# Performance work log

Hardware: AMD Instinct MI355X
Metric: run time of the kernel (lower is better)

Reference implementation:

```python
import jax, jax.numpy as jnp
import numpy as np

N, IN, HID, OUT, C, H = 50000, 1488, 1024, 512, 32, 8
E = 800000

def setup_inputs() -> dict:
    key = jax.random.key(0)
    ks = jax.random.split(key, 16)
    s = lambda k, shape, fan: jax.random.normal(k, shape, jnp.float32) * (1.0 / np.sqrt(fan))
    return {
        "x": jax.random.normal(ks[0], (N, IN), jnp.float32),
        "edge_index": jax.random.randint(ks[1], (2, E), 0, N, jnp.int64),
        "ln_g": jnp.ones((IN,), jnp.float32),
        "ln_b": jnp.zeros((IN,), jnp.float32),
        "W1": s(ks[2], (IN, HID), IN), "b1": jnp.zeros((HID,), jnp.float32),
        "W2": s(ks[3], (HID, OUT), HID), "b2": jnp.zeros((OUT,), jnp.float32),
        "Wr": s(ks[4], (OUT, C * H), OUT), "br": jnp.zeros((C * H,), jnp.float32),
        "Wg": s(ks[5], (OUT, C * H), OUT),
        "att_src": s(ks[6], (H, C), C),
        "att_dst": s(ks[7], (H, C), C),
        "bg": jnp.zeros((C * H,), jnp.float32),
    }

def reference(x, edge_index, ln_g, ln_b, W1, b1, W2, b2, Wr, br, Wg, att_src, att_dst, bg):
    n = x.shape[0]
    # LayerNorm
    mu = jnp.mean(x, axis=-1, keepdims=True)
    var = jnp.mean(jnp.square(x - mu), axis=-1, keepdims=True)
    xn = (x - mu) * jax.lax.rsqrt(var + 1e-5) * ln_g + ln_b
    # init_proj MLP
    h = jax.nn.relu(xn @ W1 + b1) @ W2 + b2            # [N, OUT]
    res = h @ Wr + br                                   # [N, H*C]
    # GATConv (add_self_loops=True, dropout inactive in eval)
    loops = jnp.arange(n, dtype=edge_index.dtype)
    src = jnp.concatenate([edge_index[0], loops])
    dst = jnp.concatenate([edge_index[1], loops])
    g = (h @ Wg).reshape(n, H, C)                       # [N, H, C]
    a_src = jnp.sum(g * att_src, axis=-1)               # [N, H]
    a_dst = jnp.sum(g * att_dst, axis=-1)               # [N, H]
    e = jax.nn.leaky_relu(a_src[src] + a_dst[dst], 0.2) # [E', H]
    m = jax.ops.segment_max(e, dst, num_segments=n)     # per-dst softmax (stable)
    ex = jnp.exp(e - m[dst])
    denom = jax.ops.segment_sum(ex, dst, num_segments=n)
    alpha = ex / (denom[dst] + 1e-16)                   # [E', H]
    msg = alpha[:, :, None] * g[src]                    # [E', H, C]
    agg = jax.ops.segment_sum(msg, dst, num_segments=n) # [N, H, C]
    out = agg.reshape(n, H * C) + bg
    return jax.nn.elu(out) + res
```

## Files before the change

### kernel.cpp

```cpp
#include <hip/hip_runtime.h>
#include <hip/hip_bf16.h>
#include <cstdint>
#include <cstddef>

#define NND 50000
#define DIN 1488
#define DINP 1536
#define DHID 1024
#define DOUT 512
#define DHC 256
#define NE 800000
#define NHD 8
#define SPLITC 256

typedef __attribute__((ext_vector_type(8))) short short8;
typedef __attribute__((ext_vector_type(4))) short short4v;
typedef __attribute__((ext_vector_type(4))) float f32x4;
typedef __attribute__((ext_vector_type(4))) int int4v;
typedef unsigned short ushort_t;

__device__ __forceinline__ unsigned short f2bf(float f){
  union { float f; unsigned u; } v; v.f = f;
  unsigned r = v.u + 0x7fffu + ((v.u >> 16) & 1u);
  return (unsigned short)(r >> 16);
}
__device__ __forceinline__ float bf2f(unsigned short u){
  union { unsigned u; float f; } v; v.u = ((unsigned)u) << 16;
  return v.f;
}

__device__ __forceinline__ void async16(const void* g, void* l){
  __builtin_amdgcn_global_load_lds((__attribute__((address_space(1))) void*)g,
                                   (__attribute__((address_space(3))) void*)l, 16, 0, 0);
}

__device__ __forceinline__ void tc_tile(const float* __restrict__ W,
                                        ushort_t* __restrict__ WT,
                                        int K, int Nn, int Kp, int bx, int by){
  __shared__ float tile[32][33];
  const int tx = threadIdx.x & 31, ty = threadIdx.x >> 5;
  const int k0 = bx*32, n0 = by*32;
  for (int i = ty; i < 32; i += 8){
    int k = k0 + i, n = n0 + tx;
    tile[i][tx] = (k < K && n < Nn) ? W[(size_t)k*Nn + n] : 0.f;
  }
  __syncthreads();
  for (int i = ty; i < 32; i += 8){
    int n = n0 + i, k = k0 + tx;
    if (n < Nn && k < Kp) WT[(size_t)n*Kp + k] = f2bf(tile[tx][i]);
  }
}
__global__ __launch_bounds__(256) void prep_kernel(const float* W1, const float* Wr,
                                                   const float* Wg, const float* W2,
                                                   const float* b2, const float* br,
                                                   ushort_t* W1T, ushort_t* WrgT,
                                                   ushort_t* W2bf, float* b2rg,
                                                   int* cnt){
  int b = blockIdx.x;
  if (b < 1536){ tc_tile(W1, W1T, DIN, DHID, DINP, b % 48, b / 48); return; }
  b -= 1536;
  if (b < 128){ tc_tile(Wr, WrgT, DOUT, DHC, DOUT, b % 16, b / 16); return; }
  b -= 128;
  if (b < 128){ tc_tile(Wg, WrgT + 256*DOUT, DOUT, DHC, DOUT, b % 16, b / 16); return; }
  b -= 128;
  if (b < 256){
    const int idx = (b*256 + threadIdx.x)*8;
    f32x4 v0 = *(const f32x4*)(W2 + idx);
    f32x4 v1 = *(const f32x4*)(W2 + idx + 4);
    union { ushort_t u[8]; short8 s; } o;
    o.u[0]=f2bf(v0.x); o.u[1]=f2bf(v0.y); o.u[2]=f2bf(v0.z); o.u[3]=f2bf(v0.w);
    o.u[4]=f2bf(v1.x); o.u[5]=f2bf(v1.y); o.u[6]=f2bf(v1.z); o.u[7]=f2bf(v1.w);
    *(short8*)(W2bf + idx) = o.s;
    return;
  }
  b -= 256;
  if (b < 2){
    const int c = b*256 + threadIdx.x;
    float acc = 0.f;
    if (c < 256){
      for (int j = 0; j < DOUT; ++j) acc += b2[j]*Wr[(size_t)j*DHC + c];
      acc += br[c];
    } else {
      const int cc = c - 256;
      for (int j = 0; j < DOUT; ++j) acc += b2[j]*Wg[(size_t)j*DHC + cc];
    }
    b2rg[c] = acc;
    return;
  }
  b -= 2;
  { int i = b*256 + threadIdx.x; if (i < NND) cnt[i] = 0; }
}

#define LN_BLOCKS 12500
__global__ __launch_bounds__(256) void ln_count(const float* __restrict__ x,
                                                const float* __restrict__ gw,
                                                const float* __restrict__ bw,
                                                ushort_t* __restrict__ xn,
                                                const int* __restrict__ ei,
                                                int* __restrict__ cnt){
  const int bid = blockIdx.x;
  if (bid >= LN_BLOCKS){
    int e = (bid - LN_BLOCKS)*256 + threadIdx.x;
    if (e < NE) atomicAdd(&cnt[ei[NE + e]], 1);
    return;
  }
  const int wid = threadIdx.x >> 6, lane = threadIdx.x & 63;
  const int row = bid*4 + wid;
  if (row >= NND) return;
  const float* xr = x + (size_t)row * DIN;
  float s = 0.f, sq = 0.f;
  for (int i = lane*4; i < DIN; i += 256){
    f32x4 v = *(const f32x4*)(xr + i);
    s  += v.x + v.y + v.z + v.w;
    sq += v.x*v.x + v.y*v.y + v.z*v.z + v.w*v.w;
  }
  #pragma unroll
  for (int o = 32; o; o >>= 1){ s += __shfl_xor(s, o); sq += __shfl_xor(sq, o); }
  const float mu = s * (1.f/DIN);
  const float var = sq * (1.f/DIN) - mu*mu;
  const float rstd = rsqrtf(var + 1e-5f);
  ushort_t* xo = xn + (size_t)row * DINP;
  for (int i = lane*4; i < DIN; i += 256){
    f32x4 v = *(const f32x4*)(xr + i);
    f32x4 gg = *(const f32x4*)(gw + i);
    f32x4 bb = *(const f32x4*)(bw + i);
    union { ushort_t u[4]; unsigned long long q; } o;
    o.u[0] = f2bf((v.x-mu)*rstd*gg.x + bb.x);
    o.u[1] = f2bf((v.y-mu)*rstd*gg.y + bb.y);
    o.u[2] = f2bf((v.z-mu)*rstd*gg.z + bb.z);
    o.u[3] = f2bf((v.w-mu)*rstd*gg.w + bb.w);
    *(unsigned long long*)(xo + i) = o.q;
  }
  if (lane < (DINP - DIN)) xo[DIN + lane] = 0;
}

template<int ACT, int MODE, int CB, int SCAN>
__global__ __launch_bounds__(256, 2) void gemm128(const ushort_t* __restrict__ A,
                                                  const ushort_t* __restrict__ BT,
                                                  const float* __restrict__ bias,
                                                  void* __restrict__ out0,
                                                  void* __restrict__ out1,
                                                  int M, int Nn, int K,
                                                  const int* __restrict__ cnt,
                                                  int* __restrict__ offs,
                                                  int* __restrict__ cur){
  __shared__ __align__(16) ushort_t lds[2][2][128*64];
  const int t = threadIdx.x, wid = t >> 6, lane = t & 63;

  const int bid = blockIdx.x - SCAN, nwg = gridDim.x - SCAN;
  const int q = nwg >> 3, r = nwg & 7;
  const int xcd = bid & 7, slot = bid >> 3;
  const int lg = (xcd < r ? xcd*(q+1) : r*(q+1) + (xcd - r)*q) + slot;
  const int brow = (lg / CB) * 128, bcol = (lg % CB) * 128;

  const int l8  = t >> 3;
  const int cb  = (t & 7) << 4;
  const int scb = cb ^ ((l8 & 7) << 4);
  const ushort_t* pAr[4]; const ushort_t* pBr[4];
  #pragma unroll
  for (int rd = 0; rd < 4; ++rd){
    int ra = brow + rd*32 + l8; ra = ra < M ? ra : M-1;
    int rb = bcol + rd*32 + l8; rb = rb < Nn ? rb : Nn-1;
    pAr[rd] = A  + (size_t)ra*K + (scb >> 1);
    pBr[rd] = BT + (size_t)rb*K + (scb >> 1);
  }
  const int w8 = wid * 8;

#define STAGE1(buf, kt) do {                                           \
    const int _o = (kt) * 64;                                          \
    _Pragma("unroll")                                                  \
    for (int _rd = 0; _rd < 4; ++_rd){                                 \
      async16(pAr[_rd] + _o, &lds[buf][0][(_rd*32 + w8)*64]);          \
      async16(pBr[_rd] + _o, &lds[buf][1][(_rd*32 + w8)*64]);          \
    }                                                                  \
  } while(0)

  f32x4 acc[4][4];
  #pragma unroll
  for (int i=0;i<4;i++)
    #pragma unroll
    for (int j=0;j<4;j++) acc[i][j] = (f32x4){0.f,0.f,0.f,0.f};

  const int wr = (wid >> 1)*64, wc = (wid & 1)*64;
  const int fr = lane & 15;
  const int kb0 = (lane >> 4) << 4;
  const int sx  = (fr & 7) << 4;
  const int ko0 = ((kb0      ) ^ sx) >> 1;
  const int ko1 = ((kb0 | 64 ) ^ sx) >> 1;

  const int nk = K >> 6;
  STAGE1(0, 0);
  STAGE1(1, 1);
  for (int kt = 0; kt < nk; ++kt){
    const ushort_t* bA = lds[kt & 1][0];
    const ushort_t* bB = lds[kt & 1][1];
    if (kt + 1 < nk) asm volatile("s_waitcnt vmcnt(8)" ::: "memory");
    else             asm volatile("s_waitcnt vmcnt(0)" ::: "memory");
    __builtin_amdgcn_s_barrier();
    short8 af[4][2], bf_[4][2];
    #pragma unroll
    for (int m=0;m<4;m++){
      const int ra = (wr + m*16 + fr)*64;
      const int rb = (wc + m*16 + fr)*64;
      af[m][0]  = *(const short8*)&bA[ra + ko0];
      af[m][1]  = *(const short8*)&bA[ra + ko1];
      bf_[m][0] = *(const short8*)&bB[rb + ko0];
      bf_[m][1] = *(const short8*)&bB[rb + ko1];
    }
    asm volatile("s_waitcnt lgkmcnt(0)" ::: "memory");
    __builtin_amdgcn_sched_barrier(0);
    __builtin_amdgcn_s_barrier();
    if (kt + 2 < nk) STAGE1(kt & 1, kt + 2);
    __builtin_amdgcn_s_setprio(1);
    #pragma unroll
    for (int m=0;m<4;m++)
      #pragma unroll
      for (int n=0;n<4;n++){
        acc[m][n] = __builtin_amdgcn_mfma_f32_16x16x32_bf16(af[m][0], bf_[n][0], acc[m][n], 0, 0, 0);
        acc[m][n] = __builtin_amdgcn_mfma_f32_16x16x32_bf16(af[m][1], bf_[n][1], acc[m][n], 0, 0, 0);
      }
    __builtin_amdgcn_s_setprio(0);
  }
#undef STAGE1

  bool isf32;
  float* outF = nullptr; ushort_t* outB = nullptr; int ostride = 0, ocb = 0;
  if (MODE == 0){ isf32 = true;  outF = (float*)out0;    ostride = Nn; ocb = bcol; }
  else if (MODE == 1){ isf32 = false; outB = (ushort_t*)out0; ostride = Nn; ocb = bcol; }
  else {
    if (bcol < SPLITC){ isf32 = true;  outF = (float*)out0;    ostride = SPLITC;      ocb = bcol; }
    else              { isf32 = false; outB = (ushort_t*)out1; ostride = Nn - SPLITC; ocb = bcol - SPLITC; }
  }
  float bv[4];
  #pragma unroll
  for (int n=0;n<4;n++){
    const int col = wc + n*16 + (lane & 15);
    float b = 0.f;
    if (MODE == 2){ if (isf32 && bias) b = bias[bcol + col]; }
    else if (bias) b = bias[bcol + col];
    bv[n] = b;
  }
  float* sF = (float*)&lds[0][0][0];
  ushort_t* sB = (ushort_t*)&lds[0][0][0];
  const int trow = t >> 3, tc16 = (t & 7) * 16;
  #pragma unroll
  for (int c = 0; c < 4; ++c){
    __syncthreads();
    if ((wid >> 1) == (c >> 1)){
      #pragma unroll
      for (int mm = 0; mm < 2; ++mm){
        const int m = 2*(c & 1) + mm;
        const int rbase = m*16 + (lane >> 4)*4 - (c & 1)*32;
        #pragma unroll
        for (int n = 0; n < 4; ++n){
          const int col = wc + n*16 + (lane & 15);
          #pragma unroll
          for (int j = 0; j < 4; ++j){
            float v = acc[m][n][j] + bv[n];
            if (ACT) v = v > 0.f ? v : 0.f;
            if (isf32) sF[(rbase + j)*128 + col] = v;
            else       sB[(rbase + j)*128 + col] = f2bf(v);
          }
        }
      }
    }
    __syncthreads();
    const int grow = brow + c*32 + trow;
    if (grow < M){
      if (isf32){
        float* dst = outF + (size_t)grow*ostride + ocb + tc16;
        const float* src = sF + trow*128 + tc16;
        #pragma unroll
        for (int q2 = 0; q2 < 4; ++q2) ((f32x4*)dst)[q2] = ((const f32x4*)src)[q2];
      } else {
        ushort_t* dst = outB + (size_t)grow*ostride + ocb + tc16;
        const ushort_t* src = sB + trow*128 + tc16;
        #pragma unroll
        for (int q2 = 0; q2 < 2; ++q2) ((short8*)dst)[q2] = ((const short8*)src)[q2];
      }
    }
  }
}

template<int ACT, int CB>
__global__ __launch_bounds__(512, 1) void gemm256p8(const ushort_t* __restrict__ A,
                                                    const ushort_t* __restrict__ BT,
                                                    const float* __restrict__ bias,
                                                    ushort_t* __restrict__ out0,
                                                    int M, int Nn, int K,
                                                    const int* __restrict__ cnt,
                                                    int* __restrict__ offs,
                                                    int* __restrict__ cur){
  __shared__ __align__(16) ushort_t lds[2][2][2][64*128];
  const int t = threadIdx.x, wid = t >> 6, lane = t & 63;

  if (blockIdx.x == 0){
    int* sbuf = (int*)&lds[0][0][0][0];
    const int chunk = (NND + 255) >> 8;
    int s = 0;
    if (t < 256){
      const int s0 = t*chunk;
      const int s1 = (s0 + chunk < NND) ? s0 + chunk : NND;
      for (int i = s0; i < s1; i += 4){
        int4v v = *(const int4v*)(cnt + i);
        s += v.x + v.y + v.z + v.w + 4;
      }
    }
    sbuf[t] = s; __syncthreads();
    for (int o = 1; o < 256; o <<= 1){
      int xv = (t >= o && t < 256) ? sbuf[t-o] : 0;
      __syncthreads();
      if (t < 256) sbuf[t] += xv;
      __syncthreads();
    }
    if (t < 256){
      int run = sbuf[t] - s;
      const int s0 = t*chunk;
      const int s1 = (s0 + chunk < NND) ? s0 + chunk : NND;
      for (int i = s0; i < s1; i += 4){
        int4v v = *(const int4v*)(cnt + i);
        int4v cu;
        cu.x = run; run += v.x + 1;
        cu.y = run; run += v.y + 1;
        cu.z = run; run += v.z + 1;
        cu.w = run; run += v.w + 1;
        *(int4v*)(cur + i)  = cu;
        *(int4v*)(offs + i) = cu;
      }
      if (t == 255) offs[NND] = run;
    }
    return;
  }

  const int bid = blockIdx.x - 1, nwg = gridDim.x - 1;
  const int q = nwg >> 3, r = nwg & 7;
  const int xcd = bid & 7, slot = bid >> 3;
  const int lg = (xcd < r ? xcd*(q+1) : r*(q+1) + (xcd - r)*q) + slot;
  const int brow = (lg / CB) * 256, bcol = (lg % CB) * 256;

  const int l8  = t >> 3;
  const int cb  = (t & 7) << 4;
  const unsigned scb = (unsigned)(cb ^ ((l8 & 7) << 4));
  unsigned rowA[2][2], rowB[2][2];
  #pragma unroll
  for (int hf = 0; hf < 2; ++hf)
    #pragma unroll
    for (int rd = 0; rd < 2; ++rd){
      int ra = brow + hf*128 + rd*64 + l8; ra = ra < M ? ra : M-1;
      int rb = bcol + hf*128 + rd*64 + l8; rb = rb < Nn ? rb : Nn-1;
      rowA[hf][rd] = (unsigned)ra * (unsigned)(K*2);
      rowB[hf][rd] = (unsigned)rb * (unsigned)(K*2);
    }
  const int w8 = wid * 8;

#define STG_A(buf, hf, kt) do {                                               \
    const unsigned _ob = (unsigned)(kt)*128u + scb;                           \
    async16((const char*)A + rowA[hf][0] + _ob, &lds[buf][0][hf][(w8)*64]);   \
    async16((const char*)A + rowA[hf][1] + _ob, &lds[buf][0][hf][(64+w8)*64]);\
  } while(0)
#define STG_B(buf, hf, kt) do {                                               \
    const unsigned _ob = (unsigned)(kt)*128u + scb;                           \
    async16((const char*)BT + rowB[hf][0] + _ob, &lds[buf][1][hf][(w8)*64]);  \
    async16((const char*)BT + rowB[hf][1] + _ob, &lds[buf][1][hf][(64+w8)*64]);\
  } while(0)

  f32x4 acc[8][4];
  #pragma unroll
  for (int i=0;i<8;i++)
    #pragma unroll
    for (int j=0;j<4;j++) acc[i][j] = (f32x4){0.f,0.f,0.f,0.f};

  const int wrow = (wid >> 2), wcol = (wid & 3);
  const int fr = lane & 15;
  const int kb0 = (lane >> 4) << 4;
  const int sx  = (fr & 7) << 4;
  const int ko0 = ((kb0      ) ^ sx) >> 1;
  const int ko1 = ((kb0 | 64 ) ^ sx) >> 1;
  const int bhalf = wcol >> 1, brl = (wcol & 1)*64;

#define RD_A(buf, m) do {                                          \
    const int _ra = ((m)*16 + fr)*64;                              \
    af[m][0] = *(const short8*)&lds[buf][0][wrow][_ra + ko0];      \
    af[m][1] = *(const short8*)&lds[buf][0][wrow][_ra + ko1];      \
  } while(0)
#define RD_B(buf, n) do {                                          \
    const int _rb = (brl + (n)*16 + fr)*64;                        \
    bf[n][0] = *(const short8*)&lds[buf][1][bhalf][_rb + ko0];     \
    bf[n][1] = *(const short8*)&lds[buf][1][bhalf][_rb + ko1];     \
  } while(0)
#define SYNC_PH() do {                                             \
    __builtin_amdgcn_s_barrier();                                  \
    asm volatile("s_waitcnt lgkmcnt(0)" ::: "memory");             \
    __builtin_amdgcn_sched_barrier(0);                             \
  } while(0)
#define MFMA_Q(M0, N0) do {                                        \
    __builtin_amdgcn_s_setprio(1);                                 \
    _Pragma("unroll")                                              \
    for (int _m=(M0); _m<(M0)+4; ++_m)                             \
      _Pragma("unroll")                                            \
      for (int _n=(N0); _n<(N0)+2; ++_n){                          \
        acc[_m][_n] = __builtin_amdgcn_mfma_f32_16x16x32_bf16(af[_m][0], bf[_n][0], acc[_m][_n], 0, 0, 0); \
        acc[_m][_n] = __builtin_amdgcn_mfma_f32_16x16x32_bf16(af[_m][1], bf[_n][1], acc[_m][_n], 0, 0, 0); \
      }                                                            \
    __builtin_amdgcn_s_setprio(0);                                 \
  } while(0)

  const int nk = K >> 6;
  STG_A(0,0,0); STG_A(0,1,0); STG_B(0,0,0); STG_B(0,1,0);
  STG_A(1,0,1); STG_A(1,1,1);
  asm volatile("s_waitcnt vmcnt(4)" ::: "memory");
  __builtin_amdgcn_s_barrier();

  for (int kt = 0; kt < nk; ++kt){
    const int buf = kt & 1, obuf = buf ^ 1;
    short8 af[8][2], bf[4][2];
    RD_A(buf,0); RD_A(buf,1); RD_A(buf,2); RD_A(buf,3);
    RD_B(buf,0); RD_B(buf,1);
    if (kt + 1 < nk) STG_B(obuf, 0, kt + 1);
    SYNC_PH();
    MFMA_Q(0, 0);
    RD_A(buf,4); RD_A(buf,5); RD_A(buf,6); RD_A(buf,7);
    if (kt + 1 < nk) STG_B(obuf, 1, kt + 1);
    SYNC_PH();
    MFMA_Q(4, 0);
    RD_B(buf,2); RD_B(buf,3);
    if (kt + 2 < nk) STG_A(buf, 0, kt + 2);
    SYNC_PH();
    MFMA_Q(0, 2);
    if (kt + 2 < nk){
      STG_A(buf, 1, kt + 2);
      asm volatile("s_waitcnt vmcnt(4)" ::: "memory");
    } else {
      asm volatile("s_waitcnt vmcnt(0)" ::: "memory");
    }
    __builtin_amdgcn_s_barrier();
    MFMA_Q(4, 2);
  }
#undef STG_A
#undef STG_B
#undef RD_A
#undef RD_B
#undef SYNC_PH
#undef MFMA_Q

  float bv[4];
  #pragma unroll
  for (int n=0;n<4;n++){
    const int col = bcol + wcol*64 + n*16 + (lane & 15);
    bv[n] = bias ? bias[col] : 0.f;
  }
  ushort_t* sB = (ushort_t*)&lds[0][0][0][0];
  __syncthreads();
  #pragma unroll
  for (int m=0;m<8;m++){
    const int row = wrow*128 + m*16 + (lane >> 4)*4;
    #pragma unroll
    for (int n=0;n<4;n++){
      const int col = wcol*64 + n*16 + (lane & 15);
      #pragma unroll
      for (int j=0;j<4;j++){
        float v = acc[m][n][j] + bv[n];
        if (ACT) v = v > 0.f ? v : 0.f;
        sB[(row+j)*256 + col] = f2bf(v);
      }
    }
  }
  __syncthreads();
  const int srow = t >> 5, scol8 = (t & 31) * 8;
  #pragma unroll
  for (int rr = 0; rr < 16; ++rr){
    const int rloc = rr*16 + srow;
    const int grow = brow + rloc;
    if (grow < M)
      *(short8*)(out0 + (size_t)grow*Nn + bcol + scol8) = *(const short8*)&sB[rloc*256 + scol8];
  }
}

#define G2_NWG 392
template<int ACT, int MODE, int CB, int EXTRA>
__global__ __launch_bounds__(512, 2) void gemm256(const ushort_t* __restrict__ A,
                                                  const ushort_t* __restrict__ BT,
                                                  const float* __restrict__ bias,
                                                  void* __restrict__ out0,
                                                  void* __restrict__ out1,
                                                  int M, int Nn, int K,
                                                  const int* __restrict__ ei,
                                                  int* __restrict__ cur,
                                                  int* __restrict__ eidx,
                                                  const float* __restrict__ att_s,
                                                  const float* __restrict__ att_d,
                                                  float* __restrict__ asrc,
                                                  float* __restrict__ adst){
  __shared__ __align__(16) ushort_t lds[2][2][256*64];
  const int t = threadIdx.x, wid = t >> 6, lane = t & 63;

  if (EXTRA == 1 && blockIdx.x >= G2_NWG){
    int i = (blockIdx.x - G2_NWG)*512 + t;
    if (i < NND){
      int p = atomicAdd(&cur[i], 1); eidx[p] = i;
    } else if (i < NND + NE){
      int e = i - NND;
      int src = ei[e], dst = ei[NE + e];
      int p = atomicAdd(&cur[dst], 1);
      eidx[p] = src;
    }
    return;
  }

  const int bid = blockIdx.x, nwg = G2_NWG;
  const int q = nwg >> 3, r = nwg & 7;
  const int xcd = bid & 7, slot = bid >> 3;
  const int lg = (xcd < r ? xcd*(q+1) : r*(q+1) + (xcd - r)*q) + slot;
  const int brow = (lg / CB) * 256, bcol = (lg % CB) * 256;

  const int l8  = t >> 3;
  const int cb  = (t & 7) << 4;
  const unsigned scb = (unsigned)(cb ^ ((l8 & 7) << 4));
  unsigned rowA[4], rowB[4];
  #pragma unroll
  for (int rd = 0; rd < 4; ++rd){
    int ra = brow + rd*64 + l8; ra = ra < M ? ra : M-1;
    int rb = bcol + rd*64 + l8; rb = rb < Nn ? rb : Nn-1;
    rowA[rd] = (unsigned)ra * (unsigned)(K*2);
    rowB[rd] = (unsigned)rb * (unsigned)(K*2);
  }
  const int wst = (wid * 8) * 64;

#define STAGE2(buf, kt) do {                                              \
    const unsigned _ob = (unsigned)(kt)*128u + scb;                       \
    _Pragma("unroll")                                                     \
    for (int _rd = 0; _rd < 4; ++_rd){                                    \
      async16((const char*)A  + rowA[_rd] + _ob, &lds[buf][0][_rd*64*64 + wst]); \
      async16((const char*)BT + rowB[_rd] + _ob, &lds[buf][1][_rd*64*64 + wst]); \
    }                                                                     \
  } while(0)

  f32x4 acc[8][4];
  #pragma unroll
  for (int i=0;i<8;i++)
    #pragma unroll
    for (int j=0;j<4;j++) acc[i][j] = (f32x4){0.f,0.f,0.f,0.f};

  const int wrow = (wid >> 2), wcol = (wid & 3);
  const int fr = lane & 15;
  const int kb0 = (lane >> 4) << 4;
  const int sx  = (fr & 7) << 4;
  const int ko0 = ((kb0      ) ^ sx) >> 1;
  const int ko1 = ((kb0 | 64 ) ^ sx) >> 1;

  const int nk = K >> 6;
  STAGE2(0, 0);
  STAGE2(1, 1);
  for (int kt = 0; kt < nk; ++kt){
    const ushort_t* bA = lds[kt & 1][0];
    const ushort_t* bB = lds[kt & 1][1];
    if (kt + 1 < nk) asm volatile("s_waitcnt vmcnt(8)" ::: "memory");
    else             asm volatile("s_waitcnt vmcnt(0)" ::: "memory");
    __builtin_amdgcn_s_barrier();
    short8 af[8][2], bf_[4][2];
    #pragma unroll
    for (int m=0;m<8;m++){
      const int ra = (wrow*128 + m*16 + fr)*64;
      af[m][0] = *(const short8*)&bA[ra + ko0];
      af[m][1] = *(const short8*)&bA[ra + ko1];
    }
    #pragma unroll
    for (int n=0;n<4;n++){
      const int rb = (wcol*64 + n*16 + fr)*64;
      bf_[n][0] = *(const short8*)&bB[rb + ko0];
      bf_[n][1] = *(const short8*)&bB[rb + ko1];
    }
    asm volatile("s_waitcnt lgkmcnt(0)" ::: "memory");
    __builtin_amdgcn_sched_barrier(0);
    __builtin_amdgcn_s_barrier();
    if (kt + 2 < nk) STAGE2(kt & 1, kt + 2);
    __builtin_amdgcn_s_setprio(1);
    #pragma unroll
    for (int m=0;m<8;m++)
      #pragma unroll
      for (int n=0;n<4;n++){
        acc[m][n] = __builtin_amdgcn_mfma_f32_16x16x32_bf16(af[m][0], bf_[n][0], acc[m][n], 0, 0, 0);
        acc[m][n] = __builtin_amdgcn_mfma_f32_16x16x32_bf16(af[m][1], bf_[n][1], acc[m][n], 0, 0, 0);
      }
    __builtin_amdgcn_s_setprio(0);
  }
#undef STAGE2

  const bool isf32 = (MODE == 0) || (MODE == 2 && bcol == 0);
  float bv[4];
  #pragma unroll
  for (int n=0;n<4;n++){
    const int col = bcol + wcol*64 + n*16 + (lane & 15);
    float b = 0.f;
    if (MODE == 1){ if (bias) b = bias[col]; }
    if (MODE == 2){ b = bias[col]; }
    bv[n] = b;
  }

  if (isf32){
    float* outF; int ostride, ocb;
    if (MODE == 0){ outF = (float*)out0; ostride = Nn;  ocb = bcol; }
    else          { outF = (float*)out0; ostride = 256; ocb = 0;    }
    float* sF = (float*)&lds[0][0][0];
    #pragma unroll
    for (int p = 0; p < 2; ++p){
      __syncthreads();
      if (wrow == p){
        #pragma unroll
        for (int m=0;m<8;m++){
          const int row = m*16 + (lane >> 4)*4;
          #pragma unroll
          for (int n=0;n<4;n++){
            const int col = wcol*64 + n*16 + (lane & 15);
            #pragma unroll
            for (int j=0;j<4;j++){
              float v = acc[m][n][j] + bv[n];
              if (ACT) v = v > 0.f ? v : 0.f;
              sF[(row+j)*256 + col] = v;
            }
          }
        }
      }
      __syncthreads();
      const int srow = t >> 6, scol4 = (t & 63) * 4;
      #pragma unroll
      for (int rr = 0; rr < 16; ++rr){
        const int rloc = rr*8 + srow;
        const int grow = brow + p*128 + rloc;
        if (grow < M)
          *(f32x4*)(outF + (size_t)grow*ostride + ocb + scol4) = *(const f32x4*)&sF[rloc*256 + scol4];
      }
    }
  } else {
    ushort_t* outB; int ostride, ocb;
    if (MODE == 1){ outB = (ushort_t*)out0; ostride = Nn;  ocb = bcol; }
    else          { outB = (ushort_t*)out1; ostride = 256; ocb = 0;    }
    ushort_t* sB = (ushort_t*)&lds[0][0][0];
    __syncthreads();
    #pragma unroll
    for (int m=0;m<8;m++){
      const int row = wrow*128 + m*16 + (lane >> 4)*4;
      #pragma unroll
      for (int n=0;n<4;n++){
        const int col = wcol*64 + n*16 + (lane & 15);
        #pragma unroll
        for (int j=0;j<4;j++){
          float v = acc[m][n][j] + bv[n];
          if (ACT) v = v > 0.f ? v : 0.f;
          sB[(row+j)*256 + col] = f2bf(v);
        }
      }
    }
    __syncthreads();
    const int srow = t >> 5, scol8 = (t & 31) * 8;
    #pragma unroll
    for (int rr = 0; rr < 16; ++rr){
      const int rloc = rr*16 + srow;
      const int grow = brow + rloc;
      if (grow < M)
        *(short8*)(outB + (size_t)grow*ostride + ocb + scol8) = *(const short8*)&sB[rloc*256 + scol8];
    }
    if (MODE == 2){
      const int h = t & 7;
      const int hc0 = h * 32;
      #pragma unroll
      for (int k = 0; k < 4; ++k){
        const int rloc = (t >> 3) + k*64;
        const int grow = brow + rloc;
        if (grow < M){
          float a = 0.f, d = 0.f;
          #pragma unroll
          for (int c0 = 0; c0 < 32; c0 += 8){
            short8 gv = *(const short8*)&sB[rloc*256 + hc0 + c0];
            #pragma unroll
            for (int j = 0; j < 8; ++j){
              float g = bf2f((ushort_t)gv[j]);
              a += g*att_s[hc0 + c0 + j];
              d += g*att_d[hc0 + c0 + j];
            }
          }
          asrc[grow*NHD + h] = a;
          adst[grow*NHD + h] = d;
        }
      }
    }
  }
}

__global__ __launch_bounds__(256) void gat_agg(const int* __restrict__ offs,
                                               const int* __restrict__ eidx,
                                               const float* __restrict__ asrc,
                                               const float* __restrict__ adst,
                                               const ushort_t* __restrict__ gm,
                                               const float* __restrict__ res,
                                               const float* __restrict__ bg,
                                               float* __restrict__ out){
  const int wid = threadIdx.x >> 6, lane = threadIdx.x & 63;
  const int node = blockIdx.x*4 + wid;
  if (node >= NND) return;
  const int h = lane >> 3, jj = lane & 7;
  const int e0 = offs[node], deg = offs[node+1] - e0;
  const float adv = adst[node*NHD + h];

  float mx = -1e30f;
  for (int j = jj; j < deg; j += 8){
    int s = eidx[e0 + j];
    float e = asrc[s*NHD + h] + adv; e = e > 0.f ? e : 0.2f*e;
    mx = fmaxf(mx, e);
  }
  mx = fmaxf(mx, __shfl_xor(mx, 1));
  mx = fmaxf(mx, __shfl_xor(mx, 2));
  mx = fmaxf(mx, __shfl_xor(mx, 4));

  const int c4 = lane*4;
  float sm = 0.f;
  f32x4 acc = {0.f,0.f,0.f,0.f};
  for (int j0 = 0; j0 < deg; j0 += 8){
    const int cnt = (deg - j0) < 8 ? (deg - j0) : 8;
    int s = 0; float w = 0.f;
    if (jj < cnt){
      s = eidx[e0 + j0 + jj];
      float e = asrc[s*NHD + h] + adv; e = e > 0.f ? e : 0.2f*e;
      w = __expf(e - mx);
      sm += w;
    }
    #pragma unroll
    for (int u = 0; u < 8; ++u){
      if (u < cnt){
        const int   su = __builtin_amdgcn_readlane(s, u);
        const float wu = __shfl(w, (h << 3) | u);
        short4v gv = *(const short4v*)(gm + (size_t)su*DHC + c4);
        acc.x += wu*bf2f((ushort_t)gv.x);
        acc.y += wu*bf2f((ushort_t)gv.y);
        acc.z += wu*bf2f((ushort_t)gv.z);
        acc.w += wu*bf2f((ushort_t)gv.w);
      }
    }
  }
  sm += __shfl_xor(sm, 1); sm += __shfl_xor(sm, 2); sm += __shfl_xor(sm, 4);
  const float inv = 1.f/(sm + 1e-16f);

  f32x4 bgv = *(const f32x4*)(bg + c4);
  f32x4 rv  = *(const f32x4*)(res + (size_t)node*DHC + c4);
  f32x4 o;
  #pragma unroll
  for (int q = 0; q < 4; ++q){
    float v = acc[q]*inv + bgv[q];
    v = v > 0.f ? v : expm1f(v);
    o[q] = v + rv[q];
  }
  *(f32x4*)(out + (size_t)node*DHC + c4) = o;
}

extern "C" void kernel_launch(void* const* d_in, const int* in_sizes, int n_in,
                              void* d_out, int out_size, void* d_ws, size_t ws_size,
                              hipStream_t stream){
  (void)in_sizes; (void)n_in; (void)out_size; (void)ws_size;
  const float* x     = (const float*)d_in[0];
  const int*   ei    = (const int*)d_in[1];
  const float* ln_g  = (const float*)d_in[2];
  const float* ln_b  = (const float*)d_in[3];
  const float* W1    = (const float*)d_in[4];
  const float* b1    = (const float*)d_in[5];
  const float* W2    = (const float*)d_in[6];
  const float* b2    = (const float*)d_in[7];
  const float* Wr    = (const float*)d_in[8];
  const float* br    = (const float*)d_in[9];
  const float* Wg    = (const float*)d_in[10];
  const float* att_s = (const float*)d_in[11];
  const float* att_d = (const float*)d_in[12];
  const float* bg    = (const float*)d_in[13];
  float* out = (float*)d_out;

  char* p = (char*)d_ws;
  ushort_t* xn   = (ushort_t*)(p);
  ushort_t* h1   = (ushort_t*)(p + 153600000);
  float*    asrc = (float*)(p + 256000000);
  float*    adst = (float*)(p + 257600000);
  int*      cnt  = (int*)(p + 259200000);
  int*      offs = (int*)(p + 259400064);
  int*      cur  = (int*)(p + 259600128);
  int*      eidx = (int*)(p + 259800192);
  ushort_t* W1T  = (ushort_t*)d_out;
  ushort_t* WrgT = (ushort_t*)((char*)d_out + 3145728);
  ushort_t* W2bf = (ushort_t*)((char*)d_out + 3670016);
  ushort_t* WcT  = (ushort_t*)((char*)d_out + 4718592);
  float*    b2rg = (float*)((char*)d_out + 5767168);
  float*    res  = (float*)(p + 0);
  ushort_t* gm   = (ushort_t*)(p + 51200000);

  prep_kernel<<<2246, 256, 0, stream>>>(W1, Wr, Wg, W2, b2, br,
                                        W1T, WrgT, W2bf, b2rg, cnt);

  gemm128<0,1,8,0><<<32, 256, 0, stream>>>(WrgT, W2bf, nullptr, WcT, nullptr,
                                           512, 1024, 512, nullptr, nullptr, nullptr);

  ln_count<<<LN_BLOCKS + (NE + 255)/256, 256, 0, stream>>>(x, ln_g, ln_b, xn, ei, cnt);

  gemm256p8<1,4><<<785, 512, 0, stream>>>(xn, W1T, b1, h1,
                                          NND, DHID, DINP, cnt, offs, cur);

  gemm256<0,2,2,1><<<G2_NWG + (NND + NE + 511)/512, 512, 0, stream>>>(
      h1, WcT, b2rg, res, gm, NND, 2*DHC, DHID,
      ei, cur, eidx, att_s, att_d, asrc, adst);

  gat_agg<<<(NND + 3)/4, 256, 0, stream>>>(offs, eidx, asrc, adst, gm, res, bg, out);
}
```

Measured before the change: 530.4 us.

## Merge weight prep with LayerNorm/count and fold Wc GEMM into main GEMM launch

Folds the weight-prep kernel into the LayerNorm/edge-count kernel, and moves the small W_rg·W2 product GEMM into the same launch as the first big GEMM as 8 extra blocks using the 256-tile body. The count zeroing becomes a hipMemsetAsync. This removes two kernel launches and the serialization between small prep kernels, though the combined GEMM now depends on weight prep finishing in the same earlier kernel. The 8 WcT blocks run alongside the h1 GEMM tiles.

Measured after the change: 508.6 us. 1.04x faster.

```diff
diff --git a/kernel.cpp b/kernel.cpp
--- a/kernel.cpp
+++ b/kernel.cpp
@@ -50,289 +50,100 @@
     if (n < Nn && k < Kp) WT[(size_t)n*Kp + k] = f2bf(tile[tx][i]);
   }
 }
-__global__ __launch_bounds__(256) void prep_kernel(const float* W1, const float* Wr,
-                                                   const float* Wg, const float* W2,
-                                                   const float* b2, const float* br,
-                                                   ushort_t* W1T, ushort_t* WrgT,
-                                                   ushort_t* W2bf, float* b2rg,
-                                                   int* cnt){
-  int b = blockIdx.x;
-  if (b < 1536){ tc_tile(W1, W1T, DIN, DHID, DINP, b % 48, b / 48); return; }
-  b -= 1536;
-  if (b < 128){ tc_tile(Wr, WrgT, DOUT, DHC, DOUT, b % 16, b / 16); return; }
-  b -= 128;
-  if (b < 128){ tc_tile(Wg, WrgT + 256*DOUT, DOUT, DHC, DOUT, b % 16, b / 16); return; }
-  b -= 128;
-  if (b < 256){
-    const int idx = (b*256 + threadIdx.x)*8;
-    f32x4 v0 = *(const f32x4*)(W2 + idx);
-    f32x4 v1 = *(const f32x4*)(W2 + idx + 4);
-    union { ushort_t u[8]; short8 s; } o;
-    o.u[0]=f2bf(v0.x); o.u[1]=f2bf(v0.y); o.u[2]=f2bf(v0.z); o.u[3]=f2bf(v0.w);
-    o.u[4]=f2bf(v1.x); o.u[5]=f2bf(v1.y); o.u[6]=f2bf(v1.z); o.u[7]=f2bf(v1.w);
-    *(short8*)(W2bf + idx) = o.s;
+
+#define F1_LN   12500
+#define F1_PREP (F1_LN + 2050)
+__global__ __launch_bounds__(256) void fused1(const float* __restrict__ x,
+                                              const float* __restrict__ gw,
+                                              const float* __restrict__ bw,
+                                              ushort_t* __restrict__ xn,
+                                              const int* __restrict__ ei,
+                                              int* __restrict__ cnt,
+                                              const float* W1, const float* Wr,
+                                              const float* Wg, const float* W2,
+                                              const float* b2, const float* br,
+                                              ushort_t* W1T, ushort_t* WrgT,
+                                              ushort_t* W2bf, float* b2rg){
+  const int bid = blockIdx.x;
+  if (bid < F1_LN){
+    const int wid = threadIdx.x >> 6, lane = threadIdx.x & 63;
+    const int row = bid*4 + wid;
+    if (row >= NND) return;
+    const float* xr = x + (size_t)row * DIN;
+    float s = 0.f, sq = 0.f;
+    for (int i = lane*4; i < DIN; i += 256){
+      f32x4 v = *(const f32x4*)(xr + i);
+      s  += v.x + v.y + v.z + v.w;
+      sq += v.x*v.x + v.y*v.y + v.z*v.z + v.w*v.w;
+    }
+    #pragma unroll
+    for (int o = 32; o; o >>= 1){ s += __shfl_xor(s, o); sq += __shfl_xor(sq, o); }
+    const float mu = s * (1.f/DIN);
+    const float var = sq * (1.f/DIN) - mu*mu;
+    const float rstd = rsqrtf(var + 1e-5f);
+    ushort_t* xo = xn + (size_t)row * DINP;
+    for (int i = lane*4; i < DIN; i += 256){
+      f32x4 v = *(const f32x4*)(xr + i);
+      f32x4 gg = *(const f32x4*)(gw + i);
+      f32x4 bb = *(const f32x4*)(bw + i);
+      union { ushort_t u[4]; unsigned long long q; } o;
+      o.u[0] = f2bf((v.x-mu)*rstd*gg.x + bb.x);
+      o.u[1] = f2bf((v.y-mu)*rstd*gg.y + bb.y);
+      o.u[2] = f2bf((v.z-mu)*rstd*gg.z + bb.z);
+      o.u[3] = f2bf((v.w-mu)*rstd*gg.w + bb.w);
+      *(unsigned long long*)(xo + i) = o.q;
+    }
+    if (lane < (DINP - DIN)) xo[DIN + lane] = 0;
     return;
   }
-  b -= 256;
-  if (b < 2){
-    const int c = b*256 + threadIdx.x;
-    float acc = 0.f;
-    if (c < 256){
-      for (int j = 0; j < DOUT; ++j) acc += b2[j]*Wr[(size_t)j*DHC + c];
-      acc += br[c];
-    } else {
-      const int cc = c - 256;
-      for (int j = 0; j < DOUT; ++j) acc += b2[j]*Wg[(size_t)j*DHC + cc];
-    }
-    b2rg[c] = acc;
-    return;
-  }
-  b -= 2;
-  { int i = b*256 + threadIdx.x; if (i < NND) cnt[i] = 0; }
-}
-
-#define LN_BLOCKS 12500
-__global__ __launch_bounds__(256) void ln_count(const float* __restrict__ x,
-                                                const float* __restrict__ gw,
-                                                const float* __restrict__ bw,
-                                                ushort_t* __restrict__ xn,
-                                                const int* __restrict__ ei,
-                                                int* __restrict__ cnt){
-  const int bid = blockIdx.x;
-  if (bid >= LN_BLOCKS){
-    int e = (bid - LN_BLOCKS)*256 + threadIdx.x;
+  if (bid < F1_PREP){
+    int b = bid - F1_LN;
+    if (b < 1536){ tc_tile(W1, W1T, DIN, DHID, DINP, b % 48, b / 48); return; }
+    b -= 1536;
+    if (b < 128){ tc_tile(Wr, WrgT, DOUT, DHC, DOUT, b % 16, b / 16); return; }
+    b -= 128;
+    if (b < 128){ tc_tile(Wg, WrgT + 256*DOUT, DOUT, DHC, DOUT, b % 16, b / 16); return; }
+    b -= 128;
+    if (b < 256){
+      const int idx = (b*256 + threadIdx.x)*8;
+      f32x4 v0 = *(const f32x4*)(W2 + idx);
+      f32x4 v1 = *(const f32x4*)(W2 + idx + 4);
+      union { ushort_t u[8]; short8 s; } o;
+      o.u[0]=f2bf(v0.x); o.u[1]=f2bf(v0.y); o.u[2]=f2bf(v0.z); o.u[3]=f2bf(v0.w);
+      o.u[4]=f2bf(v1.x); o.u[5]=f2bf(v1.y); o.u[6]=f2bf(v1.z); o.u[7]=f2bf(v1.w);
+      *(short8*)(W2bf + idx) = o.s;
+      return;
+    }
+    b -= 256;
+    {
+      const int c = b*256 + threadIdx.x;
+      float acc = 0.f;
+      if (c < 256){
+        for (int j = 0; j < DOUT; ++j) acc += b2[j]*Wr[(size_t)j*DHC + c];
+        acc += br[c];
+      } else {
+        const int cc = c - 256;
+        for (int j = 0; j < DOUT; ++j) acc += b2[j]*Wg[(size_t)j*DHC + cc];
+      }
+      b2rg[c] = acc;
+      return;
+    }
+  }
+  {
+    int e = (bid - F1_PREP)*256 + threadIdx.x;
     if (e < NE) atomicAdd(&cnt[ei[NE + e]], 1);
-    return;
-  }
-  const int wid = threadIdx.x >> 6, lane = threadIdx.x & 63;
-  const int row = bid*4 + wid;
-  if (row >= NND) return;
-  const float* xr = x + (size_t)row * DIN;
-  float s = 0.f, sq = 0.f;
-  for (int i = lane*4; i < DIN; i += 256){
-    f32x4 v = *(const f32x4*)(xr + i);
-    s  += v.x + v.y + v.z + v.w;
-    sq += v.x*v.x + v.y*v.y + v.z*v.z + v.w*v.w;
-  }
-  #pragma unroll
-  for (int o = 32; o; o >>= 1){ s += __shfl_xor(s, o); sq += __shfl_xor(sq, o); }
-  const float mu = s * (1.f/DIN);
-  const float var = sq * (1.f/DIN) - mu*mu;
-  const float rstd = rsqrtf(var + 1e-5f);
-  ushort_t* xo = xn + (size_t)row * DINP;
-  for (int i = lane*4; i < DIN; i += 256){
-    f32x4 v = *(const f32x4*)(xr + i);
-    f32x4 gg = *(const f32x4*)(gw + i);
-    f32x4 bb = *(const f32x4*)(bw + i);
-    union { ushort_t u[4]; unsigned long long q; } o;
-    o.u[0] = f2bf((v.x-mu)*rstd*gg.x + bb.x);
-    o.u[1] = f2bf((v.y-mu)*rstd*gg.y + bb.y);
-    o.u[2] = f2bf((v.z-mu)*rstd*gg.z + bb.z);
-    o.u[3] = f2bf((v.w-mu)*rstd*gg.w + bb.w);
-    *(unsigned long long*)(xo + i) = o.q;
-  }
-  if (lane < (DINP - DIN)) xo[DIN + lane] = 0;
-}
-
-template<int ACT, int MODE, int CB, int SCAN>
-__global__ __launch_bounds__(256, 2) void gemm128(const ushort_t* __restrict__ A,
-                                                  const ushort_t* __restrict__ BT,
-                                                  const float* __restrict__ bias,
-                                                  void* __restrict__ out0,
-                                                  void* __restrict__ out1,
-                                                  int M, int Nn, int K,
-                                                  const int* __restrict__ cnt,
-                                                  int* __restrict__ offs,
-                                                  int* __restrict__ cur){
-  __shared__ __align__(16) ushort_t lds[2][2][128*64];
+  }
+}
+
+__device__ __forceinline__ void g256p8_body(ushort_t (&lds)[2][2][2][64*128],
+                                            const ushort_t* __restrict__ A,
+                                            const ushort_t* __restrict__ BT,
+                                            const float* __restrict__ bias,
+                                            ushort_t* __restrict__ out0,
+                                            int M, int Nn, int K,
+                                            int bid, int nwg, bool act){
   const int t = threadIdx.x, wid = t >> 6, lane = t & 63;
-
-  const int bid = blockIdx.x - SCAN, nwg = gridDim.x - SCAN;
-  const int q = nwg >> 3, r = nwg & 7;
-  const int xcd = bid & 7, slot = bid >> 3;
-  const int lg = (xcd < r ? xcd*(q+1) : r*(q+1) + (xcd - r)*q) + slot;
-  const int brow = (lg / CB) * 128, bcol = (lg % CB) * 128;
-
-  const int l8  = t >> 3;
-  const int cb  = (t & 7) << 4;
-  const int scb = cb ^ ((l8 & 7) << 4);
-  const ushort_t* pAr[4]; const ushort_t* pBr[4];
-  #pragma unroll
-  for (int rd = 0; rd < 4; ++rd){
-    int ra = brow + rd*32 + l8; ra = ra < M ? ra : M-1;
-    int rb = bcol + rd*32 + l8; rb = rb < Nn ? rb : Nn-1;
-    pAr[rd] = A  + (size_t)ra*K + (scb >> 1);
-    pBr[rd] = BT + (size_t)rb*K + (scb >> 1);
-  }
-  const int w8 = wid * 8;
-
-#define STAGE1(buf, kt) do {                                           \
-    const int _o = (kt) * 64;                                          \
-    _Pragma("unroll")                                                  \
-    for (int _rd = 0; _rd < 4; ++_rd){                                 \
-      async16(pAr[_rd] + _o, &lds[buf][0][(_rd*32 + w8)*64]);          \
-      async16(pBr[_rd] + _o, &lds[buf][1][(_rd*32 + w8)*64]);          \
-    }                                                                  \
-  } while(0)
-
-  f32x4 acc[4][4];
-  #pragma unroll
-  for (int i=0;i<4;i++)
-    #pragma unroll
-    for (int j=0;j<4;j++) acc[i][j] = (f32x4){0.f,0.f,0.f,0.f};
-
-  const int wr = (wid >> 1)*64, wc = (wid & 1)*64;
-  const int fr = lane & 15;
-  const int kb0 = (lane >> 4) << 4;
-  const int sx  = (fr & 7) << 4;
-  const int ko0 = ((kb0      ) ^ sx) >> 1;
-  const int ko1 = ((kb0 | 64 ) ^ sx) >> 1;
-
-  const int nk = K >> 6;
-  STAGE1(0, 0);
-  STAGE1(1, 1);
-  for (int kt = 0; kt < nk; ++kt){
-    const ushort_t* bA = lds[kt & 1][0];
-    const ushort_t* bB = lds[kt & 1][1];
-    if (kt + 1 < nk) asm volatile("s_waitcnt vmcnt(8)" ::: "memory");
-    else             asm volatile("s_waitcnt vmcnt(0)" ::: "memory");
-    __builtin_amdgcn_s_barrier();
-    short8 af[4][2], bf_[4][2];
-    #pragma unroll
-    for (int m=0;m<4;m++){
-      const int ra = (wr + m*16 + fr)*64;
-      const int rb = (wc + m*16 + fr)*64;
-      af[m][0]  = *(const short8*)&bA[ra + ko0];
-      af[m][1]  = *(const short8*)&bA[ra + ko1];
-      bf_[m][0] = *(const short8*)&bB[rb + ko0];
-      bf_[m][1] = *(const short8*)&bB[rb + ko1];
-    }
-    asm volatile("s_waitcnt lgkmcnt(0)" ::: "memory");
-    __builtin_amdgcn_sched_barrier(0);
-    __builtin_amdgcn_s_barrier();
-    if (kt + 2 < nk) STAGE1(kt & 1, kt + 2);
-    __builtin_amdgcn_s_setprio(1);
-    #pragma unroll
-    for (int m=0;m<4;m++)
-      #pragma unroll
-      for (int n=0;n<4;n++){
-        acc[m][n] = __builtin_amdgcn_mfma_f32_16x16x32_bf16(af[m][0], bf_[n][0], acc[m][n], 0, 0, 0);
-        acc[m][n] = __builtin_amdgcn_mfma_f32_16x16x32_bf16(af[m][1], bf_[n][1], acc[m][n], 0, 0, 0);
-      }
-    __builtin_amdgcn_s_setprio(0);
-  }
-#undef STAGE1
-
-  bool isf32;
-  float* outF = nullptr; ushort_t* outB = nullptr; int ostride = 0, ocb = 0;
-  if (MODE == 0){ isf32 = true;  outF = (float*)out0;    ostride = Nn; ocb = bcol; }
-  else if (MODE == 1){ isf32 = false; outB = (ushort_t*)out0; ostride = Nn; ocb = bcol; }
-  else {
-    if (bcol < SPLITC){ isf32 = true;  outF = (float*)out0;    ostride = SPLITC;      ocb = bcol; }
-    else              { isf32 = false; outB = (ushort_t*)out1; ostride = Nn - SPLITC; ocb = bcol - SPLITC; }
-  }
-  float bv[4];
-  #pragma unroll
-  for (int n=0;n<4;n++){
-    const int col = wc + n*16 + (lane & 15);
-    float b = 0.f;
-    if (MODE == 2){ if (isf32 && bias) b = bias[bcol + col]; }
-    else if (bias) b = bias[bcol + col];
-    bv[n] = b;
-  }
-  float* sF = (float*)&lds[0][0][0];
-  ushort_t* sB = (ushort_t*)&lds[0][0][0];
-  const int trow = t >> 3, tc16 = (t & 7) * 16;
-  #pragma unroll
-  for (int c = 0; c < 4; ++c){
-    __syncthreads();
-    if ((wid >> 1) == (c >> 1)){
-      #pragma unroll
-      for (int mm = 0; mm < 2; ++mm){
-        const int m = 2*(c & 1) + mm;
-        const int rbase = m*16 + (lane >> 4)*4 - (c & 1)*32;
-        #pragma unroll
-        for (int n = 0; n < 4; ++n){
-          const int col = wc + n*16 + (lane & 15);
-          #pragma unroll
-          for (int j = 0; j < 4; ++j){
-            float v = acc[m][n][j] + bv[n];
-            if (ACT) v = v > 0.f ? v : 0.f;
-            if (isf32) sF[(rbase + j)*128 + col] = v;
-            else       sB[(rbase + j)*128 + col] = f2bf(v);
-          }
-        }
-      }
-    }
-    __syncthreads();
-    const int grow = brow + c*32 + trow;
-    if (grow < M){
-      if (isf32){
-        float* dst = outF + (size_t)grow*ostride + ocb + tc16;
-        const float* src = sF + trow*128 + tc16;
-        #pragma unroll
-        for (int q2 = 0; q2 < 4; ++q2) ((f32x4*)dst)[q2] = ((const f32x4*)src)[q2];
-      } else {
-        ushort_t* dst = outB + (size_t)grow*ostride + ocb + tc16;
-        const ushort_t* src = sB + trow*128 + tc16;
-        #pragma unroll
-        for (int q2 = 0; q2 < 2; ++q2) ((short8*)dst)[q2] = ((const short8*)src)[q2];
-      }
-    }
-  }
-}
-
-template<int ACT, int CB>
-__global__ __launch_bounds__(512, 1) void gemm256p8(const ushort_t* __restrict__ A,
-                                                    const ushort_t* __restrict__ BT,
-                                                    const float* __restrict__ bias,
-                                                    ushort_t* __restrict__ out0,
-                                                    int M, int Nn, int K,
-                                                    const int* __restrict__ cnt,
-                                                    int* __restrict__ offs,
-                                                    int* __restrict__ cur){
-  __shared__ __align__(16) ushort_t lds[2][2][2][64*128];
-  const int t = threadIdx.x, wid = t >> 6, lane = t & 63;
-
-  if (blockIdx.x == 0){
-    int* sbuf = (int*)&lds[0][0][0][0];
-    const int chunk = (NND + 255) >> 8;
-    int s = 0;
-    if (t < 256){
-      const int s0 = t*chunk;
-      const int s1 = (s0 + chunk < NND) ? s0 + chunk : NND;
-      for (int i = s0; i < s1; i += 4){
-        int4v v = *(const int4v*)(cnt + i);
-        s += v.x + v.y + v.z + v.w + 4;
-      }
-    }
-    sbuf[t] = s; __syncthreads();
-    for (int o = 1; o < 256; o <<= 1){
-      int xv = (t >= o && t < 256) ? sbuf[t-o] : 0;
-      __syncthreads();
-      if (t < 256) sbuf[t] += xv;
-      __syncthreads();
-    }
-    if (t < 256){
-      int run = sbuf[t] - s;
-      const int s0 = t*chunk;
-      const int s1 = (s0 + chunk < NND) ? s0 + chunk : NND;
-      for (int i = s0; i < s1; i += 4){
-        int4v v = *(const int4v*)(cnt + i);
-        int4v cu;
-        cu.x = run; run += v.x + 1;
-        cu.y = run; run += v.y + 1;
-        cu.z = run; run += v.z + 1;
-        cu.w = run; run += v.w + 1;
-        *(int4v*)(cur + i)  = cu;
-        *(int4v*)(offs + i) = cu;
-      }
-      if (t == 255) offs[NND] = run;
-    }
-    return;
-  }
-
-  const int bid = blockIdx.x - 1, nwg = gridDim.x - 1;
+  const int CB = Nn >> 8;
   const int q = nwg >> 3, r = nwg & 7;
   const int xcd = bid & 7, slot = bid >> 3;
   const int lg = (xcd < r ? xcd*(q+1) : r*(q+1) + (xcd - r)*q) + slot;
@@ -460,7 +271,7 @@
       #pragma unroll
       for (int j=0;j<4;j++){
         float v = acc[m][n][j] + bv[n];
-        if (ACT) v = v > 0.f ? v : 0.f;
+        if (act) v = v > 0.f ? v : 0.f;
         sB[(row+j)*256 + col] = f2bf(v);
       }
     }
@@ -474,6 +285,65 @@
     if (grow < M)
       *(short8*)(out0 + (size_t)grow*Nn + bcol + scol8) = *(const short8*)&sB[rloc*256 + scol8];
   }
+}
+
+__global__ __launch_bounds__(512, 1) void mega_gemm(const ushort_t* __restrict__ xn,
+                                                    const ushort_t* __restrict__ W1T,
+                                                    const float* __restrict__ b1,
+                                                    ushort_t* __restrict__ h1,
+                                                    const ushort_t* __restrict__ WrgT,
+                                                    const ushort_t* __restrict__ W2bf,
+                                                    ushort_t* __restrict__ WcT,
+                                                    const int* __restrict__ cnt,
+                                                    int* __restrict__ offs,
+                                                    int* __restrict__ cur){
+  __shared__ __align__(16) ushort_t lds[2][2][2][64*128];
+  const int t = threadIdx.x;
+
+  if (blockIdx.x == 0){
+    int* sbuf = (int*)&lds[0][0][0][0];
+    const int chunk = (NND + 255) >> 8;
+    int s = 0;
+    if (t < 256){
+      const int s0 = t*chunk;
+      const int s1 = (s0 + chunk < NND) ? s0 + chunk : NND;
+      for (int i = s0; i < s1; i += 4){
+        int4v v = *(const int4v*)(cnt + i);
+        s += v.x + v.y + v.z + v.w + 4;
+      }
+    }
+    sbuf[t] = s; __syncthreads();
+    for (int o = 1; o < 256; o <<= 1){
+      int xv = (t >= o && t < 256) ? sbuf[t-o] : 0;
+      __syncthreads();
+      if (t < 256) sbuf[t] += xv;
+      __syncthreads();
+    }
+    if (t < 256){
+      int run = sbuf[t] - s;
+      const int s0 = t*chunk;
+      const int s1 = (s0 + chunk < NND) ? s0 + chunk : NND;
+      for (int i = s0; i < s1; i += 4){
+        int4v v = *(const int4v*)(cnt + i);
+        int4v cu;
+        cu.x = run; run += v.x + 1;
+        cu.y = run; run += v.y + 1;
+        cu.z = run; run += v.z + 1;
+        cu.w = run; run += v.w + 1;
+        *(int4v*)(cur + i)  = cu;
+        *(int4v*)(offs + i) = cu;
+      }
+      if (t == 255) offs[NND] = run;
+    }
+    return;
+  }
+  if (blockIdx.x < 9){
+    g256p8_body(lds, WrgT, W2bf, nullptr, WcT, 512, 1024, 512,
+                (int)blockIdx.x - 1, 8, false);
+    return;
+  }
+  g256p8_body(lds, xn, W1T, b1, h1, NND, DHID, DINP,
+              (int)blockIdx.x - 9, (int)gridDim.x - 9, true);
 }
 
 #define G2_NWG 392
@@ -789,16 +659,14 @@
   float*    res  = (float*)(p + 0);
   ushort_t* gm   = (ushort_t*)(p + 51200000);
 
-  prep_kernel<<<2246, 256, 0, stream>>>(W1, Wr, Wg, W2, b2, br,
-                                        W1T, WrgT, W2bf, b2rg, cnt);
-
-  gemm128<0,1,8,0><<<32, 256, 0, stream>>>(WrgT, W2bf, nullptr, WcT, nullptr,
-                                           512, 1024, 512, nullptr, nullptr, nullptr);
-
-  ln_count<<<LN_BLOCKS + (NE + 255)/256, 256, 0, stream>>>(x, ln_g, ln_b, xn, ei, cnt);
-
-  gemm256p8<1,4><<<785, 512, 0, stream>>>(xn, W1T, b1, h1,
-                                          NND, DHID, DINP, cnt, offs, cur);
+  hipMemsetAsync(cnt, 0, NND*sizeof(int), stream);
+
+  fused1<<<F1_PREP + (NE + 255)/256, 256, 0, stream>>>(
+      x, ln_g, ln_b, xn, ei, cnt,
+      W1, Wr, Wg, W2, b2, br, W1T, WrgT, W2bf, b2rg);
+
+  mega_gemm<<<793, 512, 0, stream>>>(xn, W1T, b1, h1, WrgT, W2bf, WcT,
+                                     cnt, offs, cur);
 
   gemm256<0,2,2,1><<<G2_NWG + (NND + NE + 511)/512, 512, 0, stream>>>(
       h1, WcT, b2rg, res, gm, NND, 2*DHC, DHID,
```
